# Performance work log

Measured on AMD Instinct MI355X. Metric: run time of the kernel, lower is better.

Reference implementation:

```python
import jax, jax.numpy as jnp
import numpy as np

B, T, D, NH = 2, 2048, 1024, 32
HD = D // NH  # 32
EPS = 1e-6


def rms_norm(x):
    # normalize over head dim in fp32, cast back
    ms = jnp.mean(x.astype(jnp.float32) ** 2, axis=-1, keepdims=True)
    return x * jax.lax.rsqrt(ms + EPS).astype(x.dtype)


def apply_rope(x, cos, sin):
    d = x.shape[-1] // 2
    x1, x2 = x[..., :d], x[..., d:]
    c = cos[: x.shape[-2], :d]
    s = sin[: x.shape[-2], :d]
    return jnp.concatenate([x1 * c - x2 * s, x2 * c + x1 * s], axis=-1)


def setup_inputs() -> dict:
    key = jax.random.key(0)
    ks = jax.random.split(key, 5)
    sc = 1.0 / np.sqrt(D)
    x = jax.random.normal(ks[0], (B, T, D), jnp.float32)
    Wq = jax.random.normal(ks[1], (D, D), jnp.float32) * sc
    Wk = jax.random.normal(ks[2], (NH * HD, D), jnp.float32) * sc
    Wv = jax.random.normal(ks[3], (NH * HD, D), jnp.float32) * sc
    Wproj = jax.random.normal(ks[4], (D, D), jnp.float32) * sc
    q_gain = jnp.ones((NH,), jnp.float32)  # qk_gain = 1.0
    # real RoPE tables, shape [T, HD//2]
    pos = np.arange(T, dtype=np.float32)
    inv = 1.0 / (10000.0 ** (np.arange(HD // 2, dtype=np.float32) / (HD // 2)))
    ang = pos[:, None] * inv[None, :]
    cos = jnp.asarray(np.cos(ang), jnp.float32)
    sin = jnp.asarray(np.sin(ang), jnp.float32)
    return {"x": x, "Wq": Wq, "Wk": Wk, "Wv": Wv, "Wproj": Wproj,
            "q_gain": q_gain, "cos": cos, "sin": sin}


def reference(x, Wq, Wk, Wv, Wproj, q_gain, cos, sin):
    Bx, Tx, Dx = x.shape
    nh = q_gain.shape[0]
    hd = Dx // nh
    # projections -> [B, H, T, hd]
    q = (x @ Wq.T).reshape(Bx, Tx, nh, hd).transpose(0, 2, 1, 3)
    k = (x @ Wk.T).reshape(Bx, Tx, nh, hd).transpose(0, 2, 1, 3)
    v = (x @ Wv.T).reshape(Bx, Tx, nh, hd).transpose(0, 2, 1, 3)
    q = apply_rope(rms_norm(q), cos, sin) * q_gain[None, :, None, None]
    k = apply_rope(rms_norm(k), cos, sin)
    scale = hd ** (-0.5)
    scores = jnp.einsum('bhqd,bhkd->bhqk', q, k) * scale
    causal = jnp.tril(jnp.ones((Tx, Tx), bool))
    scores = jnp.where(causal, scores, jnp.finfo(scores.dtype).min)
    attn = jax.nn.softmax(scores, axis=-1)
    y = jnp.einsum('bhqk,bhkd->bhqd', attn, v)
    y = y.transpose(0, 2, 1, 3).reshape(Bx, Tx, Dx)
    return y @ Wproj.T
```

## Files before the change

### kernel.cpp

```cpp
#include <hip/hip_runtime.h>

#define DEV __device__ __forceinline__

typedef __bf16 bf16x8 __attribute__((ext_vector_type(8)));
typedef float f32x4 __attribute__((ext_vector_type(4)));
typedef float f32x16 __attribute__((ext_vector_type(16)));
typedef unsigned int u32x2 __attribute__((ext_vector_type(2)));

static constexpr int Tn = 2048;
static constexpr int Dn = 1024;
static constexpr int NHn = 32;
static constexpr int Mn = 2 * Tn;
static constexpr float QSCALE = 0.17677669529663687f * 1.4426950408889634f;

DEV unsigned short f2bf(float f) {
    return __builtin_bit_cast(unsigned short, (__bf16)f);
}

DEV unsigned pkbf(float lo, float hi) {
    unsigned short l = __builtin_bit_cast(unsigned short, (__bf16)lo);
    unsigned short h = __builtin_bit_cast(unsigned short, (__bf16)hi);
    return (unsigned)l | ((unsigned)h << 16);
}

#define GPTR(p) ((const __attribute__((address_space(1))) void*)(p))
#define LPTR(p) ((__attribute__((address_space(3))) void*)(p))

__global__ __launch_bounds__(256) void cast_all(
    const float* __restrict__ x, const float* __restrict__ Wq, const float* __restrict__ Wk,
    const float* __restrict__ Wv, const float* __restrict__ Wp,
    unsigned short* __restrict__ xb, unsigned short* __restrict__ wall) {
    int i = blockIdx.x * 256 + threadIdx.x;
    const float* src;
    ushort4* dst;
    if (i < (1 << 20)) {
        src = x + (size_t)i * 4;
        dst = reinterpret_cast<ushort4*>(xb) + i;
    } else {
        int j = i - (1 << 20);
        int sel = j >> 18, off = j & ((1 << 18) - 1);
        const float* w = (sel == 0) ? Wq : (sel == 1) ? Wk : (sel == 2) ? Wv : Wp;
        src = w + (size_t)off * 4;
        dst = reinterpret_cast<ushort4*>(wall) + ((size_t)sel << 18) + off;
    }
    float4 v = *reinterpret_cast<const float4*>(src);
    ushort4 o;
    o.x = f2bf(v.x); o.y = f2bf(v.y); o.z = f2bf(v.z); o.w = f2bf(v.w);
    *dst = o;
}

__global__ __launch_bounds__(256) void gemm_qkv(
    const unsigned short* __restrict__ A, const unsigned short* __restrict__ Wall,
    unsigned short* __restrict__ Qn, unsigned short* __restrict__ Kn, unsigned short* __restrict__ Vt,
    const float* __restrict__ gain, const float* __restrict__ cosp, const float* __restrict__ sinp) {
    const int z = blockIdx.z;
    const unsigned short* Bm = Wall + (size_t)z * (Dn * Dn);
    const int m0 = blockIdx.x * 128, n0 = blockIdx.y * 128;
    const int tid = threadIdx.x, w = tid >> 6, l = tid & 63;
    const int wm = w & 1, wn = w >> 1, lm = l & 15, quad = l >> 4;

    __shared__ __align__(16) unsigned short As[128 * 32];
    __shared__ __align__(16) unsigned short Bs[128 * 32];

    f32x4 acc[4][4] = {};

    const int r0 = (w * 2 + 0) * 16 + (l >> 2);
    const int r1 = (w * 2 + 1) * 16 + (l >> 2);
    const int c0 = (l & 3) * 8;
    const unsigned short* gA0 = A + (long)(m0 + r0) * Dn + c0;
    const unsigned short* gA1 = A + (long)(m0 + r1) * Dn + c0;
    const unsigned short* gB0 = Bm + (long)(n0 + r0) * Dn + c0;
    const unsigned short* gB1 = Bm + (long)(n0 + r1) * Dn + c0;
    unsigned short* lA0 = As + (w * 2 + 0) * 16 * 32;
    unsigned short* lA1 = As + (w * 2 + 1) * 16 * 32;
    unsigned short* lB0 = Bs + (w * 2 + 0) * 16 * 32;
    unsigned short* lB1 = Bs + (w * 2 + 1) * 16 * 32;

    for (int kk = 0; kk < Dn; kk += 32) {
        __builtin_amdgcn_global_load_lds(GPTR(gA0 + kk), LPTR(lA0), 16, 0, 0);
        __builtin_amdgcn_global_load_lds(GPTR(gA1 + kk), LPTR(lA1), 16, 0, 0);
        __builtin_amdgcn_global_load_lds(GPTR(gB0 + kk), LPTR(lB0), 16, 0, 0);
        __builtin_amdgcn_global_load_lds(GPTR(gB1 + kk), LPTR(lB1), 16, 0, 0);
        __syncthreads();
        bf16x8 af[4], bfv[4];
#pragma unroll
        for (int mt = 0; mt < 4; ++mt)
            af[mt] = __builtin_bit_cast(bf16x8,
                *reinterpret_cast<const uint4*>(As + (wm * 64 + mt * 16 + lm) * 32 + quad * 8));
#pragma unroll
        for (int nt = 0; nt < 4; ++nt)
            bfv[nt] = __builtin_bit_cast(bf16x8,
                *reinterpret_cast<const uint4*>(Bs + (wn * 64 + nt * 16 + lm) * 32 + quad * 8));
#pragma unroll
        for (int mt = 0; mt < 4; ++mt)
#pragma unroll
            for (int nt = 0; nt < 4; ++nt)
                acc[mt][nt] = __builtin_amdgcn_mfma_f32_16x16x32_bf16(af[mt], bfv[nt], acc[mt][nt], 0, 0, 0);
        __syncthreads();
    }

    if (z == 2) {
#pragma unroll
        for (int mt = 0; mt < 4; ++mt) {
            int row0 = m0 + wm * 64 + mt * 16 + quad * 4;
            int b_ = row0 >> 11, t_ = row0 & (Tn - 1);
#pragma unroll
            for (int nt = 0; nt < 4; ++nt) {
                int col = n0 + wn * 64 + nt * 16 + lm;
                int hh = col >> 5, dd = col & 31;
                ushort4 o4;
                o4.x = f2bf(acc[mt][nt][0]); o4.y = f2bf(acc[mt][nt][1]);
                o4.z = f2bf(acc[mt][nt][2]); o4.w = f2bf(acc[mt][nt][3]);
                *reinterpret_cast<ushort4*>(&Vt[((long)(b_ * NHn + hh) * 32 + dd) * Tn + t_]) = o4;
            }
        }
    } else {
        unsigned short* dst = z ? Kn : Qn;
#pragma unroll
        for (int mt = 0; mt < 4; ++mt)
#pragma unroll
            for (int r = 0; r < 4; ++r) {
                int row = m0 + wm * 64 + mt * 16 + quad * 4 + r;
                int b_ = row >> 11, t_ = row & (Tn - 1);
                float c = cosp[t_ * 16 + lm], s = sinp[t_ * 16 + lm];
#pragma unroll
                for (int g = 0; g < 2; ++g) {
                    float x1 = acc[mt][2 * g][r], x2 = acc[mt][2 * g + 1][r];
                    float ssv = x1 * x1 + x2 * x2;
#pragma unroll
                    for (int off = 8; off >= 1; off >>= 1) ssv += __shfl_xor(ssv, off, 16);
                    float rinv = rsqrtf(ssv * (1.0f / 32.0f) + 1e-6f);
                    x1 *= rinv; x2 *= rinv;
                    float o1 = x1 * c - x2 * s;
                    float o2 = x2 * c + x1 * s;
                    int hh = (n0 + wn * 64 + g * 32) >> 5;
                    if (z == 0) { float gs = gain[hh] * QSCALE; o1 *= gs; o2 *= gs; }
                    long base = ((long)(b_ * NHn + hh) * Tn + t_) * 32;
                    dst[base + lm] = f2bf(o1);
                    dst[base + 16 + lm] = f2bf(o2);
                }
            }
    }
}

__global__ __launch_bounds__(256) void gemm_proj(
    const unsigned short* __restrict__ A, const unsigned short* __restrict__ Bm,
    float* __restrict__ C) {
    const int m0 = blockIdx.x * 128, n0 = blockIdx.y * 128;
    const int tid = threadIdx.x, w = tid >> 6, l = tid & 63;
    const int wm = w & 1, wn = w >> 1, lm = l & 15, quad = l >> 4;

    __shared__ __align__(16) unsigned short As[128 * 32];
    __shared__ __align__(16) unsigned short Bs[128 * 32];

    f32x4 acc[4][4] = {};

    const int r0 = (w * 2 + 0) * 16 + (l >> 2);
    const int r1 = (w * 2 + 1) * 16 + (l >> 2);
    const int c0 = (l & 3) * 8;
    const unsigned short* gA0 = A + (long)(m0 + r0) * Dn + c0;
    const unsigned short* gA1 = A + (long)(m0 + r1) * Dn + c0;
    const unsigned short* gB0 = Bm + (long)(n0 + r0) * Dn + c0;
    const unsigned short* gB1 = Bm + (long)(n0 + r1) * Dn + c0;
    unsigned short* lA0 = As + (w * 2 + 0) * 16 * 32;
    unsigned short* lA1 = As + (w * 2 + 1) * 16 * 32;
    unsigned short* lB0 = Bs + (w * 2 + 0) * 16 * 32;
    unsigned short* lB1 = Bs + (w * 2 + 1) * 16 * 32;

    for (int kk = 0; kk < Dn; kk += 32) {
        __builtin_amdgcn_global_load_lds(GPTR(gA0 + kk), LPTR(lA0), 16, 0, 0);
        __builtin_amdgcn_global_load_lds(GPTR(gA1 + kk), LPTR(lA1), 16, 0, 0);
        __builtin_amdgcn_global_load_lds(GPTR(gB0 + kk), LPTR(lB0), 16, 0, 0);
        __builtin_amdgcn_global_load_lds(GPTR(gB1 + kk), LPTR(lB1), 16, 0, 0);
        __syncthreads();
        bf16x8 af[4], bfv[4];
#pragma unroll
        for (int mt = 0; mt < 4; ++mt)
            af[mt] = __builtin_bit_cast(bf16x8,
                *reinterpret_cast<const uint4*>(As + (wm * 64 + mt * 16 + lm) * 32 + quad * 8));
#pragma unroll
        for (int nt = 0; nt < 4; ++nt)
            bfv[nt] = __builtin_bit_cast(bf16x8,
                *reinterpret_cast<const uint4*>(Bs + (wn * 64 + nt * 16 + lm) * 32 + quad * 8));
#pragma unroll
        for (int mt = 0; mt < 4; ++mt)
#pragma unroll
            for (int nt = 0; nt < 4; ++nt)
                acc[mt][nt] = __builtin_amdgcn_mfma_f32_16x16x32_bf16(af[mt], bfv[nt], acc[mt][nt], 0, 0, 0);
        __syncthreads();
    }
#pragma unroll
    for (int mt = 0; mt < 4; ++mt)
#pragma unroll
        for (int nt = 0; nt < 4; ++nt)
#pragma unroll
            for (int r = 0; r < 4; ++r) {
                int rg = m0 + wm * 64 + mt * 16 + quad * 4 + r;
                int cg = n0 + wn * 64 + nt * 16 + lm;
                C[(long)rg * Dn + cg] = acc[mt][nt][r];
            }
}

__global__ __launch_bounds__(256) void attn(
    const unsigned short* __restrict__ Qn, const unsigned short* __restrict__ Kn,
    const unsigned short* __restrict__ Vt, unsigned short* __restrict__ Y) {
    const int bx = blockIdx.x, h = blockIdx.y, b = blockIdx.z;
    const int tid = threadIdx.x, w = tid >> 6, l = tid & 63;
    const int lr = l & 31, hf = l >> 5;
    const long bh = b * NHn + h;
    const unsigned short* Qh = Qn + bh * Tn * 32;
    const unsigned short* Kh = Kn + bh * Tn * 32;
    const unsigned short* Vh = Vt + bh * 32 * Tn;

    for (int pass = 0; pass < 2; ++pass) {
        const int qb = pass ? (15 - bx) : bx;
        const int q0 = qb * 128 + w * 32;

        bf16x8 qf[2];
        qf[0] = __builtin_bit_cast(bf16x8,
            *reinterpret_cast<const uint4*>(Qh + (q0 + lr) * 32 + hf * 8));
        qf[1] = __builtin_bit_cast(bf16x8,
            *reinterpret_cast<const uint4*>(Qh + (q0 + lr) * 32 + 16 + hf * 8));
        float ss = 0.f;
#pragma unroll
        for (int j = 0; j < 8; ++j) {
            float v0 = (float)qf[0][j], v1 = (float)qf[1][j];
            ss += v0 * v0 + v1 * v1;
        }
        ss += __shfl_xor(ss, 32);
        const float Mv = __builtin_sqrtf(ss * 32.0f);
        f32x16 negC;
#pragma unroll
        for (int i = 0; i < 16; ++i) negC[i] = -Mv;

        float lsum = 0.f;
        f32x16 o = {};

        const int kend = q0 + 31;
        uint4 ka[4], va[4], kb[4], vb[4];

        auto load_t = [&](uint4* kd, uint4* vd, int k0) {
#pragma unroll
            for (int i = 0; i < 4; ++i)
                kd[i] = *reinterpret_cast<const uint4*>(
                    Kh + (k0 + (i >> 1) * 32 + lr) * 32 + (i & 1) * 16 + hf * 8);
#pragma unroll
            for (int i = 0; i < 4; ++i)
                vd[i] = *reinterpret_cast<const uint4*>(
                    Vh + lr * Tn + k0 + i * 16 + hf * 8);
        };

        auto compute_t = [&](const uint4* kd, const uint4* vd, int k0) {
#pragma unroll
            for (int sub = 0; sub < 2; ++sub) {
                const int ks = k0 + sub * 32;
                if (ks > kend) continue;
                f32x16 st = __builtin_amdgcn_mfma_f32_32x32x16_bf16(
                    __builtin_bit_cast(bf16x8, kd[sub * 2 + 0]), qf[0], negC, 0, 0, 0);
                st = __builtin_amdgcn_mfma_f32_32x32x16_bf16(
                    __builtin_bit_cast(bf16x8, kd[sub * 2 + 1]), qf[1], st, 0, 0, 0);
                const bool full = (ks + 31) <= q0;
                const int qrow = q0 + lr;
                float p[16];
#pragma unroll
                for (int r = 0; r < 16; ++r) {
                    float pv = __builtin_amdgcn_exp2f(st[r]);
                    if (!full) {
                        int kg = ks + (r & 3) + 8 * (r >> 2) + 4 * hf;
                        pv = (kg <= qrow) ? pv : 0.0f;
                    }
                    p[r] = pv;
                }
                float t0 = (p[0] + p[1]) + (p[2] + p[3]);
                float t1 = (p[4] + p[5]) + (p[6] + p[7]);
                float t2 = (p[8] + p[9]) + (p[10] + p[11]);
                float t3 = (p[12] + p[13]) + (p[14] + p[15]);
                lsum += (t0 + t1) + (t2 + t3);
                unsigned A0 = pkbf(p[0], p[1]), A1 = pkbf(p[2], p[3]);
                unsigned B0 = pkbf(p[4], p[5]), B1 = pkbf(p[6], p[7]);
                unsigned A2 = pkbf(p[8], p[9]), A3 = pkbf(p[10], p[11]);
                unsigned B2 = pkbf(p[12], p[13]), B3 = pkbf(p[14], p[15]);
                u32x2 s0 = __builtin_amdgcn_permlane32_swap(A0, B0, false, false);
                u32x2 s1 = __builtin_amdgcn_permlane32_swap(A1, B1, false, false);
                u32x2 s2 = __builtin_amdgcn_permlane32_swap(A2, B2, false, false);
                u32x2 s3 = __builtin_amdgcn_permlane32_swap(A3, B3, false, false);
                uint4 f0; f0.x = s0[0]; f0.y = s1[0]; f0.z = s0[1]; f0.w = s1[1];
                uint4 f1; f1.x = s2[0]; f1.y = s3[0]; f1.z = s2[1]; f1.w = s3[1];
                o = __builtin_amdgcn_mfma_f32_32x32x16_bf16(
                    __builtin_bit_cast(bf16x8, f0),
                    __builtin_bit_cast(bf16x8, vd[sub * 2 + 0]), o, 0, 0, 0);
                o = __builtin_amdgcn_mfma_f32_32x32x16_bf16(
                    __builtin_bit_cast(bf16x8, f1),
                    __builtin_bit_cast(bf16x8, vd[sub * 2 + 1]), o, 0, 0, 0);
            }
        };

        load_t(ka, va, 0);
        int k0 = 0;
        while (true) {
            int nk = k0 + 64;
            if (nk <= kend) load_t(kb, vb, nk);
            compute_t(ka, va, k0);
            if (nk > kend) break;
            k0 = nk;
            nk = k0 + 64;
            if (nk <= kend) load_t(ka, va, nk);
            compute_t(kb, vb, k0);
            if (nk > kend) break;
            k0 = nk;
        }

        lsum += __shfl_xor(lsum, 32);
        const float inv = 1.0f / lsum;
#pragma unroll
        for (int r = 0; r < 16; ++r) {
            int qr = (r & 3) + 8 * (r >> 2) + 4 * hf;
            float invr = __shfl(inv, qr);
            long base = ((long)(b * Tn + q0 + qr) * NHn + h) * 32;
            Y[base + lr] = f2bf(o[r] * invr);
        }
    }
}

extern "C" void kernel_launch(void* const* d_in, const int* in_sizes, int n_in,
                              void* d_out, int out_size, void* d_ws, size_t ws_size,
                              hipStream_t stream) {
    (void)in_sizes; (void)n_in; (void)out_size; (void)ws_size;
    const float* x = (const float*)d_in[0];
    const float* Wq = (const float*)d_in[1];
    const float* Wk = (const float*)d_in[2];
    const float* Wv = (const float*)d_in[3];
    const float* Wp = (const float*)d_in[4];
    const float* gain = (const float*)d_in[5];
    const float* cosp = (const float*)d_in[6];
    const float* sinp = (const float*)d_in[7];

    char* ws = (char*)d_ws;
    const size_t SZ = (size_t)Mn * Dn * 2;
    unsigned short* xb = (unsigned short*)ws;
    unsigned short* wall = (unsigned short*)(ws + SZ);
    unsigned short* qn = (unsigned short*)(ws + 2 * SZ);
    unsigned short* kn = qn + (size_t)Mn * Dn;
    unsigned short* vt = kn + (size_t)Mn * Dn;
    unsigned short* ybuf = vt + (size_t)Mn * Dn;

    cast_all<<<8192, 256, 0, stream>>>(x, Wq, Wk, Wv, Wp, xb, wall);

    gemm_qkv<<<dim3(Mn / 128, Dn / 128, 3), 256, 0, stream>>>(
        xb, wall, qn, kn, vt, gain, cosp, sinp);

    attn<<<dim3(8, NHn, 2), 256, 0, stream>>>(qn, kn, vt, ybuf);

    gemm_proj<<<dim3(Mn / 128, Dn / 128), 256, 0, stream>>>(
        ybuf, wall + (size_t)3 * Dn * Dn, (float*)d_out);
}
```

Baseline: 241.0 us.

## Stage K/V tiles through swizzled LDS with async global-to-LDS loads

The attention kernel now has the whole 256-thread block cooperatively stage each 64-key K and V tile into double-buffered shared memory using global_load_lds, instead of every wave loading its own K/V fragments into registers from global memory. The four waves share each staged tile, which cuts redundant global traffic and register pressure. Rotating swizzles are meant to avoid LDS bank conflicts. In exchange it adds a block-wide __syncthreads per tile and makes every wave iterate to the block's last key tile, which costs waves with early causal ends idle barrier time.

After: 227.4 us. 1.06x faster.

```diff
diff --git a/kernel.cpp b/kernel.cpp
--- a/kernel.cpp
+++ b/kernel.cpp
@@ -212,6 +212,16 @@
     const unsigned short* Kh = Kn + bh * Tn * 32;
     const unsigned short* Vh = Vt + bh * 32 * Tn;
 
+    __shared__ __align__(16) unsigned short KT[2][2048];
+    __shared__ __align__(16) unsigned short VT[2][2048];
+
+    const int k_row = w * 16 + (l >> 2);
+    const int k_s = ((l & 3) - (k_row >> 1)) & 3;
+    const unsigned short* ksrc = Kh + k_row * 32 + k_s * 8;
+    const int v_row = w * 8 + (l >> 3);
+    const int v_s = ((l & 7) - v_row) & 7;
+    const unsigned short* vsrc = Vh + (long)v_row * Tn + v_s * 8;
+
     for (int pass = 0; pass < 2; ++pass) {
         const int qb = pass ? (15 - bx) : bx;
         const int q0 = qb * 128 + w * 32;
@@ -237,28 +247,27 @@
         f32x16 o = {};
 
         const int kend = q0 + 31;
-        uint4 ka[4], va[4], kb[4], vb[4];
-
-        auto load_t = [&](uint4* kd, uint4* vd, int k0) {
-#pragma unroll
-            for (int i = 0; i < 4; ++i)
-                kd[i] = *reinterpret_cast<const uint4*>(
-                    Kh + (k0 + (i >> 1) * 32 + lr) * 32 + (i & 1) * 16 + hf * 8);
-#pragma unroll
-            for (int i = 0; i < 4; ++i)
-                vd[i] = *reinterpret_cast<const uint4*>(
-                    Vh + lr * Tn + k0 + i * 16 + hf * 8);
+        const int ntb = 2 * qb + 2;
+
+        auto stage = [&](int buf, int k0) {
+            __builtin_amdgcn_global_load_lds(GPTR(ksrc + k0 * 32), LPTR(&KT[buf][w * 512]), 16, 0, 0);
+            __builtin_amdgcn_global_load_lds(GPTR(vsrc + k0), LPTR(&VT[buf][w * 512]), 16, 0, 0);
         };
 
-        auto compute_t = [&](const uint4* kd, const uint4* vd, int k0) {
+        auto compute_t = [&](int buf, int k0) {
 #pragma unroll
             for (int sub = 0; sub < 2; ++sub) {
                 const int ks = k0 + sub * 32;
                 if (ks > kend) continue;
-                f32x16 st = __builtin_amdgcn_mfma_f32_32x32x16_bf16(
-                    __builtin_bit_cast(bf16x8, kd[sub * 2 + 0]), qf[0], negC, 0, 0, 0);
-                st = __builtin_amdgcn_mfma_f32_32x32x16_bf16(
-                    __builtin_bit_cast(bf16x8, kd[sub * 2 + 1]), qf[1], st, 0, 0, 0);
+                const int krow = sub * 32 + lr;
+                const int sl0 = ((0 + hf) + (krow >> 1)) & 3;
+                const int sl1 = ((2 + hf) + (krow >> 1)) & 3;
+                bf16x8 k0f = __builtin_bit_cast(bf16x8,
+                    *reinterpret_cast<const uint4*>(&KT[buf][krow * 32 + sl0 * 8]));
+                bf16x8 k1f = __builtin_bit_cast(bf16x8,
+                    *reinterpret_cast<const uint4*>(&KT[buf][krow * 32 + sl1 * 8]));
+                f32x16 st = __builtin_amdgcn_mfma_f32_32x32x16_bf16(k0f, qf[0], negC, 0, 0, 0);
+                st = __builtin_amdgcn_mfma_f32_32x32x16_bf16(k1f, qf[1], st, 0, 0, 0);
                 const bool full = (ks + 31) <= q0;
                 const int qrow = q0 + lr;
                 float p[16];
@@ -286,28 +295,27 @@
                 u32x2 s3 = __builtin_amdgcn_permlane32_swap(A3, B3, false, false);
                 uint4 f0; f0.x = s0[0]; f0.y = s1[0]; f0.z = s0[1]; f0.w = s1[1];
                 uint4 f1; f1.x = s2[0]; f1.y = s3[0]; f1.z = s2[1]; f1.w = s3[1];
+                const int slv0 = ((sub * 4 + 0 + hf) + lr) & 7;
+                const int slv1 = ((sub * 4 + 2 + hf) + lr) & 7;
+                bf16x8 v0f = __builtin_bit_cast(bf16x8,
+                    *reinterpret_cast<const uint4*>(&VT[buf][lr * 64 + slv0 * 8]));
+                bf16x8 v1f = __builtin_bit_cast(bf16x8,
+                    *reinterpret_cast<const uint4*>(&VT[buf][lr * 64 + slv1 * 8]));
                 o = __builtin_amdgcn_mfma_f32_32x32x16_bf16(
-                    __builtin_bit_cast(bf16x8, f0),
-                    __builtin_bit_cast(bf16x8, vd[sub * 2 + 0]), o, 0, 0, 0);
+                    __builtin_bit_cast(bf16x8, f0), v0f, o, 0, 0, 0);
                 o = __builtin_amdgcn_mfma_f32_32x32x16_bf16(
-                    __builtin_bit_cast(bf16x8, f1),
-                    __builtin_bit_cast(bf16x8, vd[sub * 2 + 1]), o, 0, 0, 0);
+                    __builtin_bit_cast(bf16x8, f1), v1f, o, 0, 0, 0);
             }
         };
 
-        load_t(ka, va, 0);
-        int k0 = 0;
-        while (true) {
-            int nk = k0 + 64;
-            if (nk <= kend) load_t(kb, vb, nk);
-            compute_t(ka, va, k0);
-            if (nk > kend) break;
-            k0 = nk;
-            nk = k0 + 64;
-            if (nk <= kend) load_t(ka, va, nk);
-            compute_t(kb, vb, k0);
-            if (nk > kend) break;
-            k0 = nk;
+        __syncthreads();
+        stage(0, 0);
+        int cur = 0;
+        for (int ti = 0; ti < ntb; ++ti) {
+            __syncthreads();
+            if (ti + 1 < ntb) stage(cur ^ 1, (ti + 1) * 64);
+            compute_t(cur, ti * 64);
+            cur ^= 1;
         }
 
         lsum += __shfl_xor(lsum, 32);
```
